# Kernel optimization log

Measured on AMD Instinct MI355X. Metric: run time of the kernel, lower is better.

Reference implementation:

```python
import jax, jax.numpy as jnp
import numpy as np

# ---- grid / frustum config (from default grid_config & data_config) ----
DB = (1.0, 60.0, 1.0)                 # dbound
OGH, OGW, DS = 256, 704, 16           # input size, downsample
FH, FW = OGH // DS, OGW // DS         # 16, 44
DEPTH = int(round((DB[1] - DB[0]) / DB[2]))  # 59 depth bins
NX0, NX1, NZ = 128, 128, 1            # BEV grid
DX = np.array([0.8, 0.8, 20.0], np.float32)
BX = np.array([-51.2 + 0.4, -51.2 + 0.4, 0.0], np.float32)  # row0 + dx/2


def _frustum():
    # (D, FH, FW, 3): pixel (u, v, depth)
    ds = jnp.broadcast_to(jnp.arange(DB[0], DB[1], DB[2], dtype=jnp.float32).reshape(-1, 1, 1), (DEPTH, FH, FW))
    xs = jnp.broadcast_to(jnp.linspace(0.0, OGW - 1.0, FW, dtype=jnp.float32).reshape(1, 1, FW), (DEPTH, FH, FW))
    ys = jnp.broadcast_to(jnp.linspace(0.0, OGH - 1.0, FH, dtype=jnp.float32).reshape(1, FH, 1), (DEPTH, FH, FW))
    return jnp.stack([xs, ys, ds], axis=-1)


def _geometry(rots, trans, intrins, post_rots, post_trans, bda):
    # pixel frustum -> ego-frame 3D points; (B, N, D, FH, FW, 3)
    pts = _frustum() - post_trans[:, :, None, None, None, :]
    pts = jnp.einsum('bnij,bndhwj->bndhwi', jnp.linalg.inv(post_rots), pts)
    pts = jnp.concatenate([pts[..., :2] * pts[..., 2:3], pts[..., 2:3]], axis=-1)
    comb = jnp.einsum('bnij,bnjk->bnik', rots, jnp.linalg.inv(intrins))
    pts = jnp.einsum('bnij,bndhwj->bndhwi', comb, pts) + trans[:, :, None, None, None, :]
    pts = jnp.einsum('bij,bndhwj->bndhwi', bda, pts)
    return pts


def _voxel_pool(geom, vol):
    # geom: (B,N,D,FH,FW,3), vol: (B,N,D,FH,FW,C) -> BEV (B, C*NZ, NX0, NX1)
    B, C = vol.shape[0], vol.shape[-1]
    gidx = jnp.floor((geom - (BX - DX / 2.0)) / DX).astype(jnp.int32)
    kept = ((gidx[..., 0] >= 0) & (gidx[..., 0] < NX0)
            & (gidx[..., 1] >= 0) & (gidx[..., 1] < NX1)
            & (gidx[..., 2] >= 0) & (gidx[..., 2] < NZ))
    bidx = jnp.broadcast_to(jnp.arange(B, dtype=jnp.int32).reshape(B, 1, 1, 1, 1), gidx.shape[:-1])
    flat = ((bidx * NZ + gidx[..., 2]) * NX0 + gidx[..., 0]) * NX1 + gidx[..., 1]
    nvox = B * NZ * NX0 * NX1
    flat = jnp.where(kept, flat, nvox).reshape(-1)      # dump bucket for culled pts
    feats = vol.reshape(-1, C)
    bev = jax.ops.segment_sum(feats, flat, num_segments=nvox + 1)[:nvox]
    bev = bev.reshape(B, NZ, NX0, NX1, C)
    bev = jnp.moveaxis(bev, -1, 2).reshape(B, NZ * C, NX0, NX1)  # z-major channel cat
    return bev


def setup_inputs() -> dict:
    key = jax.random.key(0)
    B, N, CIN, CT = 4, 6, 512, 64
    k1, k2 = jax.random.split(key, 2)
    x = jax.random.normal(k1, (B, N, CIN, FH, FW), dtype=jnp.float32)
    weight = jax.random.normal(k2, (DEPTH + CT, CIN), dtype=jnp.float32) * 0.02
    bias = jnp.zeros((DEPTH + CT,), dtype=jnp.float32)
    # cam->ego rotation (cam z forward -> ego x, cam x right -> ego -y, cam y down -> ego -z)
    Rcam = jnp.asarray(np.array([[0., 0., 1.], [-1., 0., 0.], [0., -1., 0.]], np.float32))
    rots = jnp.tile(Rcam, (B, N, 1, 1))
    trans = jnp.zeros((B, N, 3), dtype=jnp.float32)
    K = jnp.asarray(np.array([[600., 0., 352.], [0., 600., 128.], [0., 0., 1.]], np.float32))
    intrins = jnp.tile(K, (B, N, 1, 1))
    post_rots = jnp.tile(jnp.eye(3, dtype=jnp.float32), (B, N, 1, 1))
    post_trans = jnp.zeros((B, N, 3), dtype=jnp.float32)
    bda = jnp.tile(jnp.eye(3, dtype=jnp.float32), (B, 1, 1))
    return dict(x=x, rots=rots, trans=trans, intrins=intrins, post_rots=post_rots,
                post_trans=post_trans, bda=bda, weight=weight, bias=bias)


def reference(x, rots, trans, intrins, post_rots, post_trans, bda, weight, bias):
    # 1x1 depth/context head (eval mode): (B,N,Cin,H,W) -> (B,N,D+C,H,W)
    out = jnp.einsum('bnchw,oc->bnohw', x, weight) + bias[None, None, :, None, None]
    depth = jax.nn.softmax(out[:, :, :DEPTH], axis=2)      # (B,N,D,H,W)
    feat = out[:, :, DEPTH:]                               # (B,N,C,H,W)
    # depth-context outer product -> frustum volume (B,N,D,H,W,C)
    vol = jnp.einsum('bndhw,bnchw->bndhwc', depth, feat)
    geom = _geometry(rots, trans, intrins, post_rots, post_trans, bda)
    bev = _voxel_pool(geom, vol)                           # (B, C*NZ, 128, 128)
    return bev, depth
```

## Files before the change

### kernel.cpp

```cpp
#include <hip/hip_runtime.h>
#include <math.h>

#define CIN   512
#define NOUT  123
#define DEPN  59
#define CT    64
#define B_    4
#define N_    6
#define FH    16
#define FW    44
#define HW    704
#define NPIX  (B_*N_*HW)
#define NX    128
#define BEV_ELEMS (B_*CT*NX*NX)
#define DEPTH_OFF BEV_ELEMS

#define TDREC   40
#define WS_WB   1920
#define WS_PS   (WS_WB + 32768)
#define WS_FS   (WS_PS + NPIX*64)
#define WS_GC   (WS_FS + NPIX*64)

typedef short bf16x8 __attribute__((ext_vector_type(8)));
typedef float f32x4  __attribute__((ext_vector_type(4)));

__device__ inline unsigned short f2bf(float f) {
    unsigned u = __float_as_uint(f);
    return (unsigned short)((u + 0x7fffu + ((u >> 16) & 1u)) >> 16);
}

__device__ inline void inv3d(const double* m, double* o) {
    #pragma clang fp contract(off)
    double c00 = m[4]*m[8] - m[5]*m[7];
    double c01 = m[5]*m[6] - m[3]*m[8];
    double c02 = m[3]*m[7] - m[4]*m[6];
    double det = m[0]*c00 + m[1]*c01 + m[2]*c02;
    o[0] = c00/det; o[1] = (m[2]*m[7]-m[1]*m[8])/det; o[2] = (m[1]*m[5]-m[2]*m[4])/det;
    o[3] = c01/det; o[4] = (m[0]*m[8]-m[2]*m[6])/det; o[5] = (m[2]*m[3]-m[0]*m[5])/det;
    o[6] = c02/det; o[7] = (m[1]*m[6]-m[0]*m[7])/det; o[8] = (m[0]*m[4]-m[1]*m[3])/det;
}
__device__ inline void mm3d(const double* a, const double* b, double* o) {
    #pragma clang fp contract(off)
    for (int i = 0; i < 3; ++i)
        for (int k = 0; k < 3; ++k)
            o[i*3+k] = (a[i*3+0]*b[0*3+k] + a[i*3+1]*b[1*3+k]) + a[i*3+2]*b[2*3+k];
}

__global__ void k0_prep(const float* __restrict__ rots, const float* __restrict__ trans,
                        const float* __restrict__ intr, const float* __restrict__ prots,
                        const float* __restrict__ ptrans, const float* __restrict__ bda,
                        const float* __restrict__ W, float* __restrict__ ws,
                        float* __restrict__ dout) {
    int tid = blockIdx.x * 256 + threadIdx.x;
    int stride = gridDim.x * 256;
    float4 z = {0.f, 0.f, 0.f, 0.f};
    for (int i = tid; i < BEV_ELEMS / 4; i += stride)
        *(float4*)(dout + 4 * (size_t)i) = z;
    unsigned short* wb = (unsigned short*)(ws + WS_WB);
    for (int i = tid; i < 128 * CIN; i += stride) {
        int o = i >> 9, c = i & 511;
        wb[i] = (o < NOUT) ? f2bf(W[o * CIN + c]) : (unsigned short)0;
    }
    if (blockIdx.x == 0 && threadIdx.x < B_ * N_) {
        #pragma clang fp contract(off)
        int t = threadIdx.x;
        int b = t / N_;
        double* X = (double*)(ws) + t * TDREC;
        double PR[9], Kd[9], Rd[9], Bd[9];
        for (int i = 0; i < 9; ++i) PR[i] = (double)prots[t * 9 + i];
        for (int i = 0; i < 9; ++i) Kd[i] = (double)intr[t * 9 + i];
        for (int i = 0; i < 9; ++i) Rd[i] = (double)rots[t * 9 + i];
        for (int i = 0; i < 9; ++i) Bd[i] = (double)bda[b * 9 + i];
        double iPR[9]; inv3d(PR, iPR);
        for (int i = 0; i < 9; ++i) X[i] = iPR[i];
        for (int i = 0; i < 3; ++i) X[9 + i] = (double)ptrans[t * 3 + i];
        double iK[9];  inv3d(Kd, iK);
        double comb[9]; mm3d(Rd, iK, comb);
        for (int i = 0; i < 9; ++i) X[12 + i] = comb[i];
        for (int i = 0; i < 3; ++i) X[21 + i] = (double)trans[t * 3 + i];
        for (int i = 0; i < 9; ++i) X[24 + i] = Bd[i];
    }
}

__global__ __launch_bounds__(256) void k0b_coef(float* __restrict__ ws) {
    #pragma clang fp contract(off)
    int i = blockIdx.x * 256 + threadIdx.x;
    int b = i / (FW * 96);
    int rem = i - b * (FW * 96);
    int w = rem / 96;
    int j = rem - w * 96;
    int n = j >> 4, h = j & 15;
    const double* T = (const double*)(ws) + (b * N_ + n) * TDREC;
    const double xs = (w == 43) ? 703.0 : (double)w * (703.0 / 43.0);
    const double ys = (double)(h * 17);
    const double u0 = xs - T[9];
    const double u1 = ys - T[10];
    double pA[3], pB[3];
    #pragma unroll
    for (int k = 0; k < 3; ++k) {
        pA[k] = (T[3*k]*u0 + T[3*k+1]*u1) - T[3*k+2]*T[11];
        pB[k] = T[3*k+2];
    }
    double q0c[3] = { pA[0]*pA[2], pA[0]*pB[2] + pB[0]*pA[2], pB[0]*pB[2] };
    double q1c[3] = { pA[1]*pA[2], pA[1]*pB[2] + pB[1]*pA[2], pB[1]*pB[2] };
    double q2c[3] = { pA[2], pB[2], 0.0 };
    double rc[3][3], gc[3][3];
    #pragma unroll
    for (int r = 0; r < 3; ++r)
        #pragma unroll
        for (int k = 0; k < 3; ++k)
            rc[r][k] = ((T[12+3*r]*q0c[k] + T[13+3*r]*q1c[k]) + T[14+3*r]*q2c[k])
                       + ((k == 0) ? T[21+r] : 0.0);
    #pragma unroll
    for (int g = 0; g < 3; ++g)
        #pragma unroll
        for (int k = 0; k < 3; ++k)
            gc[g][k] = (T[24+3*g]*rc[0][k] + T[25+3*g]*rc[1][k]) + T[26+3*g]*rc[2][k];
    double* dst = (double*)(ws) + WS_GC / 2 + (size_t)i * 9;
    #pragma unroll
    for (int t = 0; t < 9; ++t) dst[t] = gc[t / 3][t % 3];
}

#define K1A   (64 * 72)
#define K1T   (K1A + 128 * 72)
__global__ __launch_bounds__(256, 2) void k1_gemm(const float* __restrict__ x,
                                                  const float* __restrict__ bias,
                                                  float* __restrict__ ws,
                                                  float* __restrict__ dout) {
    __shared__ __align__(16) unsigned short smem[2][K1T];
    const int tid = threadIdx.x;
    const int wave = tid >> 6, lane = tid & 63;
    const int l15 = lane & 15, quad = lane >> 4;
    const int bn = blockIdx.y;
    const int pixbase = blockIdx.x * 64;
    const float* xg = x + (size_t)bn * CIN * HW + pixbase;
    const unsigned short* wbg = (const unsigned short*)(ws + WS_WB);
    const int cpack = tid >> 4;
    const int pix4 = (tid & 15) * 4;
    const int wo  = tid >> 3;
    const int wsub = tid & 7;

    f32x4 acc[8] = {};
    float4 xr[2][4];
    uint4  wr[2][4];

    #pragma unroll
    for (int d = 0; d < 2; ++d) {
        const int ck = d * 64;
        const float* src = xg + (size_t)(ck + 4 * cpack) * HW + pix4;
        xr[d][0] = *(const float4*)(src);
        xr[d][1] = *(const float4*)(src + HW);
        xr[d][2] = *(const float4*)(src + 2 * HW);
        xr[d][3] = *(const float4*)(src + 3 * HW);
        #pragma unroll
        for (int i = 0; i < 4; ++i)
            wr[d][i] = *(const uint4*)(wbg + (size_t)(wo + 32 * i) * CIN + ck + wsub * 8);
    }

    #pragma unroll
    for (int it = 0; it < 8; ++it) {
        const int buf = it & 1;
        unsigned short* sa = smem[buf];
        unsigned short* sb = smem[buf] + K1A;
        {
            const float* f0 = (const float*)&xr[buf][0];
            const float* f1 = (const float*)&xr[buf][1];
            const float* f2 = (const float*)&xr[buf][2];
            const float* f3 = (const float*)&xr[buf][3];
            #pragma unroll
            for (int i = 0; i < 4; ++i) {
                uint2 pk;
                pk.x = (unsigned)f2bf(f0[i]) | ((unsigned)f2bf(f1[i]) << 16);
                pk.y = (unsigned)f2bf(f2[i]) | ((unsigned)f2bf(f3[i]) << 16);
                *(uint2*)&sa[(pix4 + i) * 72 + 4 * cpack] = pk;
            }
            #pragma unroll
            for (int i = 0; i < 4; ++i)
                *(uint4*)&sb[(wo + 32 * i) * 72 + wsub * 8] = wr[buf][i];
        }
        if (it < 6) {
            const int ck = (it + 2) * 64;
            const float* src = xg + (size_t)(ck + 4 * cpack) * HW + pix4;
            xr[buf][0] = *(const float4*)(src);
            xr[buf][1] = *(const float4*)(src + HW);
            xr[buf][2] = *(const float4*)(src + 2 * HW);
            xr[buf][3] = *(const float4*)(src + 3 * HW);
            #pragma unroll
            for (int i = 0; i < 4; ++i)
                wr[buf][i] = *(const uint4*)(wbg + (size_t)(wo + 32 * i) * CIN + ck + wsub * 8);
        }
        __syncthreads();
        #pragma unroll
        for (int ks = 0; ks < 64; ks += 32) {
            const bf16x8 a = *(const bf16x8*)&sa[(wave * 16 + l15) * 72 + ks + quad * 8];
            #pragma unroll
            for (int nt = 0; nt < 8; ++nt) {
                const bf16x8 b = *(const bf16x8*)&sb[(nt * 16 + l15) * 72 + ks + quad * 8];
                acc[nt] = __builtin_amdgcn_mfma_f32_16x16x32_bf16(a, b, acc[nt], 0, 0, 0);
            }
        }
    }

    float* sred = (float*)&smem[0][0];
    const int b = bn / N_, n = bn - b * N_;
    {
        float bb[8];
        #pragma unroll
        for (int nt = 0; nt < 8; ++nt) {
            int o = nt * 16 + l15;
            bb[nt] = (o < NOUT) ? bias[o] : 0.0f;
        }
        float* ps = ws + WS_PS;
        float* fs = ws + WS_FS;
        #pragma unroll
        for (int reg = 0; reg < 4; ++reg) {
            int pixl = wave * 16 + quad * 4 + reg;
            int pix = pixbase + pixl;
            int h = pix / FW, w = pix - h * FW;
            size_t row = (size_t)(b * FW + w) * 96 + n * FH + h;
            float v[4]; float m = -INFINITY;
            #pragma unroll
            for (int nt = 0; nt < 4; ++nt) {
                v[nt] = acc[nt][reg] + bb[nt];
                if (nt * 16 + l15 < DEPN) m = fmaxf(m, v[nt]);
            }
            #pragma unroll
            for (int msk = 8; msk >= 1; msk >>= 1) m = fmaxf(m, __shfl_xor(m, msk, 64));
            float e[4], s = 0.0f;
            #pragma unroll
            for (int nt = 0; nt < 4; ++nt) {
                e[nt] = (nt * 16 + l15 < DEPN) ? expf(v[nt] - m) : 0.0f;
                s += e[nt];
            }
            #pragma unroll
            for (int msk = 8; msk >= 1; msk >>= 1) s += __shfl_xor(s, msk, 64);
            const float inv = 1.0f / s;
            #pragma unroll
            for (int nt = 0; nt < 4; ++nt) {
                int o = nt * 16 + l15;
                if (o < DEPN) {
                    float p = e[nt] * inv;
                    ps[row * 64 + o] = p;
                    sred[pixl * 65 + o] = p;
                } else fs[row * 64 + (o - DEPN)] = v[nt];
            }
            #pragma unroll
            for (int nt = 4; nt < 8; ++nt) {
                int o = nt * 16 + l15;
                if (o < NOUT) fs[row * 64 + (o - DEPN)] = acc[nt][reg] + bb[nt];
            }
        }
    }
    __syncthreads();
    for (int o = wave; o < DEPN; o += 4)
        dout[DEPTH_OFF + ((size_t)bn * DEPN + o) * HW + pixbase + lane] = sred[lane * 65 + o];
}

#define DQ2 16
__global__ __launch_bounds__(256) void k2b_geom(float* __restrict__ ws,
                                                float* __restrict__ dout) {
    __shared__ float sF[96][64];
    __shared__ float sP[DQ2][100];
    __shared__ unsigned short sv16[DQ2 * 96];
    __shared__ __align__(16) double sG[96 * 9];
    __shared__ int sflag[DQ2];
    const int tid = threadIdx.x;
    const int bw = blockIdx.x;
    const int b = bw / FW;
    const int dbase = blockIdx.y * DQ2;
    const int nd = min(DQ2, DEPN - dbase);

    {
        const float* fsrc = ws + WS_FS + (size_t)bw * (96 * 64);
        const float* psrc = ws + WS_PS + (size_t)bw * (96 * 64);
        for (int i = tid; i < 96 * 16; i += 256) {
            int j = i >> 4, c4 = (i & 15) * 4;
            *(float4*)&sF[j][c4] = *(const float4*)(fsrc + j * 64 + c4);
        }
        for (int i = tid; i < 96 * 4; i += 256) {
            int j = i >> 2, q = i & 3;
            const float4 p4 = *(const float4*)(psrc + j * 64 + dbase + 4 * q);
            sP[4 * q + 0][j] = p4.x; sP[4 * q + 1][j] = p4.y;
            sP[4 * q + 2][j] = p4.z; sP[4 * q + 3][j] = p4.w;
        }
        const double2* gsrc = (const double2*)((const double*)(ws) + WS_GC / 2
                                               + (size_t)bw * (96 * 9));
        for (int i = tid; i < 432; i += 256)
            ((double2*)sG)[i] = gsrc[i];
    }
    __syncthreads();

    {
        const double BXY = (double)(-51.2000007629394531f);
        for (int idx = tid; idx < nd * 96; idx += 256) {
            int dl = idx / 96, j = idx - dl * 96;
            const double* G = &sG[j * 9];
            const double dsv = (double)(dbase + dl + 1);
            const double g0 = (G[2] * dsv + G[1]) * dsv + G[0];
            const double g1 = (G[5] * dsv + G[4]) * dsv + G[3];
            const double g2 = (G[8] * dsv + G[7]) * dsv + G[6];
            const double fx = floor((g0 - BXY) * 1.25);
            const double fy = floor((g1 - BXY) * 1.25);
            const bool keep = (fx >= 0.0) & (fx < 128.0) & (fy >= 0.0) & (fy < 128.0) &
                              (g2 >= -10.0) & (g2 < 10.0);
            sv16[idx] = keep ? (unsigned short)((int)fx * NX + (int)fy) : (unsigned short)0xFFFF;
        }
    }
    __syncthreads();

    {
        const int dl = tid >> 4, s = tid & 15;
        int u = -1, mix = 0;
        const int base = dl * 96 + s * 6;
        #pragma unroll
        for (int t = 0; t < 6; ++t) {
            int v = sv16[base + t];
            if (v != 0xFFFF) { if (u < 0) u = v; else if (v != u) mix = 1; }
        }
        #pragma unroll
        for (int msk = 1; msk < 16; msk <<= 1) {
            int uo = __shfl_xor(u, msk, 64);
            int mo = __shfl_xor(mix, msk, 64);
            mix = mix | mo | ((u >= 0 && uo >= 0 && uo != u) ? 1 : 0);
            u = (u < 0) ? uo : u;
        }
        if (s == 0 && dl < nd) sflag[dl] = mix ? -2 : u;
    }
    for (int idx = tid; idx < nd * 96; idx += 256) {
        if (sv16[idx] == 0xFFFF) {
            int dl = idx / 96, j = idx - dl * 96;
            sP[dl][j] = 0.0f;
        }
    }
    __syncthreads();

    const int dl = tid >> 4, ci = tid & 15;
    if (dl < nd && sflag[dl] >= 0) {
        float ax = 0.f, ay = 0.f, az = 0.f, aw = 0.f;
        for (int jj = 0; jj < 96; jj += 4) {
            const float4 pv = *(const float4*)&sP[dl][jj];
            const float4 f0 = *(const float4*)&sF[jj + 0][4 * ci];
            const float4 f1 = *(const float4*)&sF[jj + 1][4 * ci];
            const float4 f2 = *(const float4*)&sF[jj + 2][4 * ci];
            const float4 f3 = *(const float4*)&sF[jj + 3][4 * ci];
            ax = fmaf(pv.x, f0.x, ax); ay = fmaf(pv.x, f0.y, ay);
            az = fmaf(pv.x, f0.z, az); aw = fmaf(pv.x, f0.w, aw);
            ax = fmaf(pv.y, f1.x, ax); ay = fmaf(pv.y, f1.y, ay);
            az = fmaf(pv.y, f1.z, az); aw = fmaf(pv.y, f1.w, aw);
            ax = fmaf(pv.z, f2.x, ax); ay = fmaf(pv.z, f2.y, ay);
            az = fmaf(pv.z, f2.z, az); aw = fmaf(pv.z, f2.w, aw);
            ax = fmaf(pv.w, f3.x, ax); ay = fmaf(pv.w, f3.y, ay);
            az = fmaf(pv.w, f3.z, az); aw = fmaf(pv.w, f3.w, aw);
        }
        float* dst = dout + (((size_t)(b * CT + 4 * ci)) << 14) + sflag[dl];
        atomicAdd(dst,             ax);
        atomicAdd(dst + (1 << 14), ay);
        atomicAdd(dst + (2 << 14), az);
        atomicAdd(dst + (3 << 14), aw);
    }
    for (int d2 = 0; d2 < nd; ++d2) {
        if (sflag[d2] == -2) {
            int c = tid & 63, g = tid >> 6;
            for (int jj = 0; jj < 24; ++jj) {
                int j = g * 24 + jj;
                int v = sv16[d2 * 96 + j];
                if (v != 0xFFFF)
                    atomicAdd(dout + (((size_t)(b * CT + c)) << 14) + v,
                              sP[d2][j] * sF[j][c]);
            }
        }
    }
}

extern "C" void kernel_launch(void* const* d_in, const int* in_sizes, int n_in,
                              void* d_out, int out_size, void* d_ws, size_t ws_size,
                              hipStream_t stream) {
    const float* x      = (const float*)d_in[0];
    const float* rots   = (const float*)d_in[1];
    const float* trans  = (const float*)d_in[2];
    const float* intr   = (const float*)d_in[3];
    const float* prots  = (const float*)d_in[4];
    const float* ptrans = (const float*)d_in[5];
    const float* bda    = (const float*)d_in[6];
    const float* W      = (const float*)d_in[7];
    const float* bias   = (const float*)d_in[8];
    float* out = (float*)d_out;
    float* ws  = (float*)d_ws;

    k0_prep<<<512, 256, 0, stream>>>(rots, trans, intr, prots, ptrans, bda, W, ws, out);
    k0b_coef<<<66, 256, 0, stream>>>(ws);
    k1_gemm<<<dim3(HW / 64, B_ * N_), 256, 0, stream>>>(x, bias, ws, out);
    k2b_geom<<<dim3(B_ * FW, 4), 256, 0, stream>>>(ws, out);
}
```

Baseline: 163.0 us.

## Fuse all four kernels into one cooperative persistent kernel with grid syncs

Merges the prep, coefficient, GEMM and voxel-pool kernels into a single cooperative launch of 512 blocks separated by grid.sync(). The BEV zeroing moves onto the blocks left idle during the GEMM phase, the per-pixel geometry coefficients are now computed in shared memory per tile instead of round-tripping through a workspace buffer, and the GEMM prefetch goes from two-deep to one-deep register staging. The aim is to remove launch gaps and overlap the zeroing with the GEMM. In exchange it pays for grid-wide barriers and has lower occupancy limits with a single shared-memory buffer. The shallower prefetch may also expose more load latency.

Measured after the change: 274.0 us. 1.68x slower.

```diff
diff --git a/kernel.cpp b/kernel.cpp
--- a/kernel.cpp
+++ b/kernel.cpp
@@ -1,5 +1,8 @@
 #include <hip/hip_runtime.h>
+#include <hip/hip_cooperative_groups.h>
 #include <math.h>
+
+namespace cg = cooperative_groups;
 
 #define CIN   512
 #define NOUT  123
@@ -19,7 +22,10 @@
 #define WS_WB   1920
 #define WS_PS   (WS_WB + 32768)
 #define WS_FS   (WS_PS + NPIX*64)
-#define WS_GC   (WS_FS + NPIX*64)
+
+#define GRID    512
+#define K1TILES 264
+#define P2TILES (B_*FW*4)
 
 typedef short bf16x8 __attribute__((ext_vector_type(8)));
 typedef float f32x4  __attribute__((ext_vector_type(4)));
@@ -46,327 +52,324 @@
             o[i*3+k] = (a[i*3+0]*b[0*3+k] + a[i*3+1]*b[1*3+k]) + a[i*3+2]*b[2*3+k];
 }
 
-__global__ void k0_prep(const float* __restrict__ rots, const float* __restrict__ trans,
-                        const float* __restrict__ intr, const float* __restrict__ prots,
-                        const float* __restrict__ ptrans, const float* __restrict__ bda,
-                        const float* __restrict__ W, float* __restrict__ ws,
-                        float* __restrict__ dout) {
-    int tid = blockIdx.x * 256 + threadIdx.x;
-    int stride = gridDim.x * 256;
-    float4 z = {0.f, 0.f, 0.f, 0.f};
-    for (int i = tid; i < BEV_ELEMS / 4; i += stride)
-        *(float4*)(dout + 4 * (size_t)i) = z;
-    unsigned short* wb = (unsigned short*)(ws + WS_WB);
-    for (int i = tid; i < 128 * CIN; i += stride) {
-        int o = i >> 9, c = i & 511;
-        wb[i] = (o < NOUT) ? f2bf(W[o * CIN + c]) : (unsigned short)0;
+#define K1A   4608
+#define K1T   13824
+#define SMEM_BYTES 55296
+
+__global__ __launch_bounds__(256, 2) void fused(
+        const float* __restrict__ x,     const float* __restrict__ rots,
+        const float* __restrict__ trans, const float* __restrict__ intr,
+        const float* __restrict__ prots, const float* __restrict__ ptrans,
+        const float* __restrict__ bda,   const float* __restrict__ W,
+        const float* __restrict__ bias,  float* __restrict__ ws,
+        float* __restrict__ dout) {
+    __shared__ __align__(16) unsigned char smem[SMEM_BYTES];
+    cg::grid_group grid = cg::this_grid();
+    const int tid = threadIdx.x;
+    const int bid = blockIdx.x;
+
+    {
+        unsigned short* wb = (unsigned short*)(ws + WS_WB);
+        for (int i = bid * 256 + tid; i < 128 * CIN; i += GRID * 256) {
+            int o = i >> 9, c = i & 511;
+            wb[i] = (o < NOUT) ? f2bf(W[o * CIN + c]) : (unsigned short)0;
+        }
+        if (bid == 0 && tid < B_ * N_) {
+            #pragma clang fp contract(off)
+            int t = tid;
+            int b = t / N_;
+            double* X = (double*)(ws) + t * TDREC;
+            double PR[9], Kd[9], Rd[9], Bd[9];
+            for (int i = 0; i < 9; ++i) PR[i] = (double)prots[t * 9 + i];
+            for (int i = 0; i < 9; ++i) Kd[i] = (double)intr[t * 9 + i];
+            for (int i = 0; i < 9; ++i) Rd[i] = (double)rots[t * 9 + i];
+            for (int i = 0; i < 9; ++i) Bd[i] = (double)bda[b * 9 + i];
+            double iPR[9]; inv3d(PR, iPR);
+            for (int i = 0; i < 9; ++i) X[i] = iPR[i];
+            for (int i = 0; i < 3; ++i) X[9 + i] = (double)ptrans[t * 3 + i];
+            double iK[9];  inv3d(Kd, iK);
+            double comb[9]; mm3d(Rd, iK, comb);
+            for (int i = 0; i < 9; ++i) X[12 + i] = comb[i];
+            for (int i = 0; i < 3; ++i) X[21 + i] = (double)trans[t * 3 + i];
+            for (int i = 0; i < 9; ++i) X[24 + i] = Bd[i];
+        }
     }
-    if (blockIdx.x == 0 && threadIdx.x < B_ * N_) {
-        #pragma clang fp contract(off)
-        int t = threadIdx.x;
-        int b = t / N_;
-        double* X = (double*)(ws) + t * TDREC;
-        double PR[9], Kd[9], Rd[9], Bd[9];
-        for (int i = 0; i < 9; ++i) PR[i] = (double)prots[t * 9 + i];
-        for (int i = 0; i < 9; ++i) Kd[i] = (double)intr[t * 9 + i];
-        for (int i = 0; i < 9; ++i) Rd[i] = (double)rots[t * 9 + i];
-        for (int i = 0; i < 9; ++i) Bd[i] = (double)bda[b * 9 + i];
-        double iPR[9]; inv3d(PR, iPR);
-        for (int i = 0; i < 9; ++i) X[i] = iPR[i];
-        for (int i = 0; i < 3; ++i) X[9 + i] = (double)ptrans[t * 3 + i];
-        double iK[9];  inv3d(Kd, iK);
-        double comb[9]; mm3d(Rd, iK, comb);
-        for (int i = 0; i < 9; ++i) X[12 + i] = comb[i];
-        for (int i = 0; i < 3; ++i) X[21 + i] = (double)trans[t * 3 + i];
-        for (int i = 0; i < 9; ++i) X[24 + i] = Bd[i];
-    }
-}
-
-__global__ __launch_bounds__(256) void k0b_coef(float* __restrict__ ws) {
-    #pragma clang fp contract(off)
-    int i = blockIdx.x * 256 + threadIdx.x;
-    int b = i / (FW * 96);
-    int rem = i - b * (FW * 96);
-    int w = rem / 96;
-    int j = rem - w * 96;
-    int n = j >> 4, h = j & 15;
-    const double* T = (const double*)(ws) + (b * N_ + n) * TDREC;
-    const double xs = (w == 43) ? 703.0 : (double)w * (703.0 / 43.0);
-    const double ys = (double)(h * 17);
-    const double u0 = xs - T[9];
-    const double u1 = ys - T[10];
-    double pA[3], pB[3];
-    #pragma unroll
-    for (int k = 0; k < 3; ++k) {
-        pA[k] = (T[3*k]*u0 + T[3*k+1]*u1) - T[3*k+2]*T[11];
-        pB[k] = T[3*k+2];
-    }
-    double q0c[3] = { pA[0]*pA[2], pA[0]*pB[2] + pB[0]*pA[2], pB[0]*pB[2] };
-    double q1c[3] = { pA[1]*pA[2], pA[1]*pB[2] + pB[1]*pA[2], pB[1]*pB[2] };
-    double q2c[3] = { pA[2], pB[2], 0.0 };
-    double rc[3][3], gc[3][3];
-    #pragma unroll
-    for (int r = 0; r < 3; ++r)
-        #pragma unroll
-        for (int k = 0; k < 3; ++k)
-            rc[r][k] = ((T[12+3*r]*q0c[k] + T[13+3*r]*q1c[k]) + T[14+3*r]*q2c[k])
-                       + ((k == 0) ? T[21+r] : 0.0);
-    #pragma unroll
-    for (int g = 0; g < 3; ++g)
-        #pragma unroll
-        for (int k = 0; k < 3; ++k)
-            gc[g][k] = (T[24+3*g]*rc[0][k] + T[25+3*g]*rc[1][k]) + T[26+3*g]*rc[2][k];
-    double* dst = (double*)(ws) + WS_GC / 2 + (size_t)i * 9;
-    #pragma unroll
-    for (int t = 0; t < 9; ++t) dst[t] = gc[t / 3][t % 3];
-}
-
-#define K1A   (64 * 72)
-#define K1T   (K1A + 128 * 72)
-__global__ __launch_bounds__(256, 2) void k1_gemm(const float* __restrict__ x,
-                                                  const float* __restrict__ bias,
-                                                  float* __restrict__ ws,
-                                                  float* __restrict__ dout) {
-    __shared__ __align__(16) unsigned short smem[2][K1T];
-    const int tid = threadIdx.x;
-    const int wave = tid >> 6, lane = tid & 63;
-    const int l15 = lane & 15, quad = lane >> 4;
-    const int bn = blockIdx.y;
-    const int pixbase = blockIdx.x * 64;
-    const float* xg = x + (size_t)bn * CIN * HW + pixbase;
-    const unsigned short* wbg = (const unsigned short*)(ws + WS_WB);
-    const int cpack = tid >> 4;
-    const int pix4 = (tid & 15) * 4;
-    const int wo  = tid >> 3;
-    const int wsub = tid & 7;
-
-    f32x4 acc[8] = {};
-    float4 xr[2][4];
-    uint4  wr[2][4];
-
-    #pragma unroll
-    for (int d = 0; d < 2; ++d) {
-        const int ck = d * 64;
-        const float* src = xg + (size_t)(ck + 4 * cpack) * HW + pix4;
-        xr[d][0] = *(const float4*)(src);
-        xr[d][1] = *(const float4*)(src + HW);
-        xr[d][2] = *(const float4*)(src + 2 * HW);
-        xr[d][3] = *(const float4*)(src + 3 * HW);
-        #pragma unroll
-        for (int i = 0; i < 4; ++i)
-            wr[d][i] = *(const uint4*)(wbg + (size_t)(wo + 32 * i) * CIN + ck + wsub * 8);
-    }
-
-    #pragma unroll
-    for (int it = 0; it < 8; ++it) {
-        const int buf = it & 1;
-        unsigned short* sa = smem[buf];
-        unsigned short* sb = smem[buf] + K1A;
+    grid.sync();
+
+    if (bid < K1TILES) {
+        const int wave = tid >> 6, lane = tid & 63;
+        const int l15 = lane & 15, quad = lane >> 4;
+        const int bn = bid / 11;
+        const int pixbase = (bid - bn * 11) * 64;
+        const float* xg = x + (size_t)bn * CIN * HW + pixbase;
+        const unsigned short* wbg = (const unsigned short*)(ws + WS_WB);
+        const int cpack = tid >> 4;
+        const int pix4 = (tid & 15) * 4;
+        const int wo  = tid >> 3;
+        const int wsub = tid & 7;
+        unsigned short* s16 = (unsigned short*)smem;
+
+        f32x4 acc[8] = {};
+        float4 xr0, xr1, xr2, xr3;
+        uint4  wr4[4];
         {
-            const float* f0 = (const float*)&xr[buf][0];
-            const float* f1 = (const float*)&xr[buf][1];
-            const float* f2 = (const float*)&xr[buf][2];
-            const float* f3 = (const float*)&xr[buf][3];
-            #pragma unroll
-            for (int i = 0; i < 4; ++i) {
-                uint2 pk;
-                pk.x = (unsigned)f2bf(f0[i]) | ((unsigned)f2bf(f1[i]) << 16);
-                pk.y = (unsigned)f2bf(f2[i]) | ((unsigned)f2bf(f3[i]) << 16);
-                *(uint2*)&sa[(pix4 + i) * 72 + 4 * cpack] = pk;
-            }
+            const float* src = xg + (size_t)(4 * cpack) * HW + pix4;
+            xr0 = *(const float4*)(src);
+            xr1 = *(const float4*)(src + HW);
+            xr2 = *(const float4*)(src + 2 * HW);
+            xr3 = *(const float4*)(src + 3 * HW);
             #pragma unroll
             for (int i = 0; i < 4; ++i)
-                *(uint4*)&sb[(wo + 32 * i) * 72 + wsub * 8] = wr[buf][i];
-        }
-        if (it < 6) {
-            const int ck = (it + 2) * 64;
-            const float* src = xg + (size_t)(ck + 4 * cpack) * HW + pix4;
-            xr[buf][0] = *(const float4*)(src);
-            xr[buf][1] = *(const float4*)(src + HW);
-            xr[buf][2] = *(const float4*)(src + 2 * HW);
-            xr[buf][3] = *(const float4*)(src + 3 * HW);
+                wr4[i] = *(const uint4*)(wbg + (size_t)(wo + 32 * i) * CIN + wsub * 8);
+        }
+        #pragma unroll
+        for (int it = 0; it < 8; ++it) {
+            const int buf = it & 1;
+            unsigned short* sa = s16 + buf * K1T;
+            unsigned short* sb = sa + K1A;
+            {
+                const float* f0 = (const float*)&xr0; const float* f1 = (const float*)&xr1;
+                const float* f2 = (const float*)&xr2; const float* f3 = (const float*)&xr3;
+                #pragma unroll
+                for (int i = 0; i < 4; ++i) {
+                    uint2 pk;
+                    pk.x = (unsigned)f2bf(f0[i]) | ((unsigned)f2bf(f1[i]) << 16);
+                    pk.y = (unsigned)f2bf(f2[i]) | ((unsigned)f2bf(f3[i]) << 16);
+                    *(uint2*)&sa[(pix4 + i) * 72 + 4 * cpack] = pk;
+                }
+                #pragma unroll
+                for (int i = 0; i < 4; ++i)
+                    *(uint4*)&sb[(wo + 32 * i) * 72 + wsub * 8] = wr4[i];
+            }
+            if (it < 7) {
+                const int ck = (it + 1) * 64;
+                const float* src = xg + (size_t)(ck + 4 * cpack) * HW + pix4;
+                xr0 = *(const float4*)(src);
+                xr1 = *(const float4*)(src + HW);
+                xr2 = *(const float4*)(src + 2 * HW);
+                xr3 = *(const float4*)(src + 3 * HW);
+                #pragma unroll
+                for (int i = 0; i < 4; ++i)
+                    wr4[i] = *(const uint4*)(wbg + (size_t)(wo + 32 * i) * CIN + ck + wsub * 8);
+            }
+            __syncthreads();
             #pragma unroll
-            for (int i = 0; i < 4; ++i)
-                wr[buf][i] = *(const uint4*)(wbg + (size_t)(wo + 32 * i) * CIN + ck + wsub * 8);
-        }
-        __syncthreads();
-        #pragma unroll
-        for (int ks = 0; ks < 64; ks += 32) {
-            const bf16x8 a = *(const bf16x8*)&sa[(wave * 16 + l15) * 72 + ks + quad * 8];
+            for (int ks = 0; ks < 64; ks += 32) {
+                const bf16x8 a = *(const bf16x8*)&sa[(wave * 16 + l15) * 72 + ks + quad * 8];
+                #pragma unroll
+                for (int nt = 0; nt < 8; ++nt) {
+                    const bf16x8 b = *(const bf16x8*)&sb[(nt * 16 + l15) * 72 + ks + quad * 8];
+                    acc[nt] = __builtin_amdgcn_mfma_f32_16x16x32_bf16(a, b, acc[nt], 0, 0, 0);
+                }
+            }
+        }
+        float* sred = (float*)smem;
+        const int b = bn / N_, n = bn - b * N_;
+        {
+            float bb[8];
             #pragma unroll
             for (int nt = 0; nt < 8; ++nt) {
-                const bf16x8 b = *(const bf16x8*)&sb[(nt * 16 + l15) * 72 + ks + quad * 8];
-                acc[nt] = __builtin_amdgcn_mfma_f32_16x16x32_bf16(a, b, acc[nt], 0, 0, 0);
-            }
-        }
+                int o = nt * 16 + l15;
+                bb[nt] = (o < NOUT) ? bias[o] : 0.0f;
+            }
+            float* ps = ws + WS_PS;
+            float* fs = ws + WS_FS;
+            #pragma unroll
+            for (int reg = 0; reg < 4; ++reg) {
+                int pixl = wave * 16 + quad * 4 + reg;
+                int pix = pixbase + pixl;
+                int h = pix / FW, w = pix - h * FW;
+                size_t row = (size_t)(b * FW + w) * 96 + n * FH + h;
+                float v[4]; float m = -INFINITY;
+                #pragma unroll
+                for (int nt = 0; nt < 4; ++nt) {
+                    v[nt] = acc[nt][reg] + bb[nt];
+                    if (nt * 16 + l15 < DEPN) m = fmaxf(m, v[nt]);
+                }
+                #pragma unroll
+                for (int msk = 8; msk >= 1; msk >>= 1) m = fmaxf(m, __shfl_xor(m, msk, 64));
+                float e[4], s = 0.0f;
+                #pragma unroll
+                for (int nt = 0; nt < 4; ++nt) {
+                    e[nt] = (nt * 16 + l15 < DEPN) ? expf(v[nt] - m) : 0.0f;
+                    s += e[nt];
+                }
+                #pragma unroll
+                for (int msk = 8; msk >= 1; msk >>= 1) s += __shfl_xor(s, msk, 64);
+                const float inv = 1.0f / s;
+                #pragma unroll
+                for (int nt = 0; nt < 4; ++nt) {
+                    int o = nt * 16 + l15;
+                    if (o < DEPN) {
+                        float p = e[nt] * inv;
+                        ps[row * 64 + o] = p;
+                        sred[pixl * 65 + o] = p;
+                    } else fs[row * 64 + (o - DEPN)] = v[nt];
+                }
+                #pragma unroll
+                for (int nt = 4; nt < 8; ++nt) {
+                    int o = nt * 16 + l15;
+                    if (o < NOUT) fs[row * 64 + (o - DEPN)] = acc[nt][reg] + bb[nt];
+                }
+            }
+        }
+        __syncthreads();
+        for (int o = wave; o < DEPN; o += 4)
+            dout[DEPTH_OFF + ((size_t)bn * DEPN + o) * HW + pixbase + lane] = sred[lane * 65 + o];
+    } else {
+        float4 z = {0.f, 0.f, 0.f, 0.f};
+        for (int i = (bid - K1TILES) * 256 + tid; i < BEV_ELEMS / 4; i += (GRID - K1TILES) * 256)
+            *(float4*)(dout + 4 * (size_t)i) = z;
     }
-
-    float* sred = (float*)&smem[0][0];
-    const int b = bn / N_, n = bn - b * N_;
+    grid.sync();
+
     {
-        float bb[8];
-        #pragma unroll
-        for (int nt = 0; nt < 8; ++nt) {
-            int o = nt * 16 + l15;
-            bb[nt] = (o < NOUT) ? bias[o] : 0.0f;
-        }
-        float* ps = ws + WS_PS;
-        float* fs = ws + WS_FS;
-        #pragma unroll
-        for (int reg = 0; reg < 4; ++reg) {
-            int pixl = wave * 16 + quad * 4 + reg;
-            int pix = pixbase + pixl;
-            int h = pix / FW, w = pix - h * FW;
-            size_t row = (size_t)(b * FW + w) * 96 + n * FH + h;
-            float v[4]; float m = -INFINITY;
-            #pragma unroll
-            for (int nt = 0; nt < 4; ++nt) {
-                v[nt] = acc[nt][reg] + bb[nt];
-                if (nt * 16 + l15 < DEPN) m = fmaxf(m, v[nt]);
-            }
-            #pragma unroll
-            for (int msk = 8; msk >= 1; msk >>= 1) m = fmaxf(m, __shfl_xor(m, msk, 64));
-            float e[4], s = 0.0f;
-            #pragma unroll
-            for (int nt = 0; nt < 4; ++nt) {
-                e[nt] = (nt * 16 + l15 < DEPN) ? expf(v[nt] - m) : 0.0f;
-                s += e[nt];
-            }
-            #pragma unroll
-            for (int msk = 8; msk >= 1; msk >>= 1) s += __shfl_xor(s, msk, 64);
-            const float inv = 1.0f / s;
-            #pragma unroll
-            for (int nt = 0; nt < 4; ++nt) {
-                int o = nt * 16 + l15;
-                if (o < DEPN) {
-                    float p = e[nt] * inv;
-                    ps[row * 64 + o] = p;
-                    sred[pixl * 65 + o] = p;
-                } else fs[row * 64 + (o - DEPN)] = v[nt];
-            }
-            #pragma unroll
-            for (int nt = 4; nt < 8; ++nt) {
-                int o = nt * 16 + l15;
-                if (o < NOUT) fs[row * 64 + (o - DEPN)] = acc[nt][reg] + bb[nt];
-            }
-        }
-    }
-    __syncthreads();
-    for (int o = wave; o < DEPN; o += 4)
-        dout[DEPTH_OFF + ((size_t)bn * DEPN + o) * HW + pixbase + lane] = sred[lane * 65 + o];
-}
-
-#define DQ2 16
-__global__ __launch_bounds__(256) void k2b_geom(float* __restrict__ ws,
-                                                float* __restrict__ dout) {
-    __shared__ float sF[96][64];
-    __shared__ float sP[DQ2][100];
-    __shared__ unsigned short sv16[DQ2 * 96];
-    __shared__ __align__(16) double sG[96 * 9];
-    __shared__ int sflag[DQ2];
-    const int tid = threadIdx.x;
-    const int bw = blockIdx.x;
-    const int b = bw / FW;
-    const int dbase = blockIdx.y * DQ2;
-    const int nd = min(DQ2, DEPN - dbase);
-
-    {
-        const float* fsrc = ws + WS_FS + (size_t)bw * (96 * 64);
-        const float* psrc = ws + WS_PS + (size_t)bw * (96 * 64);
-        for (int i = tid; i < 96 * 16; i += 256) {
-            int j = i >> 4, c4 = (i & 15) * 4;
-            *(float4*)&sF[j][c4] = *(const float4*)(fsrc + j * 64 + c4);
-        }
-        for (int i = tid; i < 96 * 4; i += 256) {
-            int j = i >> 2, q = i & 3;
-            const float4 p4 = *(const float4*)(psrc + j * 64 + dbase + 4 * q);
-            sP[4 * q + 0][j] = p4.x; sP[4 * q + 1][j] = p4.y;
-            sP[4 * q + 2][j] = p4.z; sP[4 * q + 3][j] = p4.w;
-        }
-        const double2* gsrc = (const double2*)((const double*)(ws) + WS_GC / 2
-                                               + (size_t)bw * (96 * 9));
-        for (int i = tid; i < 432; i += 256)
-            ((double2*)sG)[i] = gsrc[i];
-    }
-    __syncthreads();
-
-    {
-        const double BXY = (double)(-51.2000007629394531f);
-        for (int idx = tid; idx < nd * 96; idx += 256) {
-            int dl = idx / 96, j = idx - dl * 96;
-            const double* G = &sG[j * 9];
-            const double dsv = (double)(dbase + dl + 1);
-            const double g0 = (G[2] * dsv + G[1]) * dsv + G[0];
-            const double g1 = (G[5] * dsv + G[4]) * dsv + G[3];
-            const double g2 = (G[8] * dsv + G[7]) * dsv + G[6];
-            const double fx = floor((g0 - BXY) * 1.25);
-            const double fy = floor((g1 - BXY) * 1.25);
-            const bool keep = (fx >= 0.0) & (fx < 128.0) & (fy >= 0.0) & (fy < 128.0) &
-                              (g2 >= -10.0) & (g2 < 10.0);
-            sv16[idx] = keep ? (unsigned short)((int)fx * NX + (int)fy) : (unsigned short)0xFFFF;
-        }
-    }
-    __syncthreads();
-
-    {
-        const int dl = tid >> 4, s = tid & 15;
-        int u = -1, mix = 0;
-        const int base = dl * 96 + s * 6;
-        #pragma unroll
-        for (int t = 0; t < 6; ++t) {
-            int v = sv16[base + t];
-            if (v != 0xFFFF) { if (u < 0) u = v; else if (v != u) mix = 1; }
-        }
-        #pragma unroll
-        for (int msk = 1; msk < 16; msk <<= 1) {
-            int uo = __shfl_xor(u, msk, 64);
-            int mo = __shfl_xor(mix, msk, 64);
-            mix = mix | mo | ((u >= 0 && uo >= 0 && uo != u) ? 1 : 0);
-            u = (u < 0) ? uo : u;
-        }
-        if (s == 0 && dl < nd) sflag[dl] = mix ? -2 : u;
-    }
-    for (int idx = tid; idx < nd * 96; idx += 256) {
-        if (sv16[idx] == 0xFFFF) {
-            int dl = idx / 96, j = idx - dl * 96;
-            sP[dl][j] = 0.0f;
-        }
-    }
-    __syncthreads();
-
-    const int dl = tid >> 4, ci = tid & 15;
-    if (dl < nd && sflag[dl] >= 0) {
-        float ax = 0.f, ay = 0.f, az = 0.f, aw = 0.f;
-        for (int jj = 0; jj < 96; jj += 4) {
-            const float4 pv = *(const float4*)&sP[dl][jj];
-            const float4 f0 = *(const float4*)&sF[jj + 0][4 * ci];
-            const float4 f1 = *(const float4*)&sF[jj + 1][4 * ci];
-            const float4 f2 = *(const float4*)&sF[jj + 2][4 * ci];
-            const float4 f3 = *(const float4*)&sF[jj + 3][4 * ci];
-            ax = fmaf(pv.x, f0.x, ax); ay = fmaf(pv.x, f0.y, ay);
-            az = fmaf(pv.x, f0.z, az); aw = fmaf(pv.x, f0.w, aw);
-            ax = fmaf(pv.y, f1.x, ax); ay = fmaf(pv.y, f1.y, ay);
-            az = fmaf(pv.y, f1.z, az); aw = fmaf(pv.y, f1.w, aw);
-            ax = fmaf(pv.z, f2.x, ax); ay = fmaf(pv.z, f2.y, ay);
-            az = fmaf(pv.z, f2.z, az); aw = fmaf(pv.z, f2.w, aw);
-            ax = fmaf(pv.w, f3.x, ax); ay = fmaf(pv.w, f3.y, ay);
-            az = fmaf(pv.w, f3.z, az); aw = fmaf(pv.w, f3.w, aw);
-        }
-        float* dst = dout + (((size_t)(b * CT + 4 * ci)) << 14) + sflag[dl];
-        atomicAdd(dst,             ax);
-        atomicAdd(dst + (1 << 14), ay);
-        atomicAdd(dst + (2 << 14), az);
-        atomicAdd(dst + (3 << 14), aw);
-    }
-    for (int d2 = 0; d2 < nd; ++d2) {
-        if (sflag[d2] == -2) {
-            int c = tid & 63, g = tid >> 6;
-            for (int jj = 0; jj < 24; ++jj) {
-                int j = g * 24 + jj;
-                int v = sv16[d2 * 96 + j];
-                if (v != 0xFFFF)
-                    atomicAdd(dout + (((size_t)(b * CT + c)) << 14) + v,
-                              sP[d2][j] * sF[j][c]);
+        float*  sF   = (float*)smem;
+        float*  sP   = (float*)(smem + 24576);
+        unsigned short* sv16 = (unsigned short*)(smem + 30976);
+        double* sG   = (double*)(smem + 34048);
+        double* sT   = (double*)(smem + 40960);
+        int*    sflag = (int*)(smem + 42880);
+
+        for (int t = bid; t < P2TILES; t += GRID) {
+            const int bw = t >> 2;
+            const int dch = t & 3;
+            const int b = bw / FW, w = bw - b * FW;
+            const int dbase = dch * 16;
+            const int nd = min(16, DEPN - dbase);
+            __syncthreads();
+
+            {
+                const float* fsrc = ws + WS_FS + (size_t)bw * (96 * 64);
+                const float* psrc = ws + WS_PS + (size_t)bw * (96 * 64);
+                for (int i = tid; i < 96 * 16; i += 256) {
+                    int j = i >> 4, c4 = (i & 15) * 4;
+                    *(float4*)&sF[j * 64 + c4] = *(const float4*)(fsrc + j * 64 + c4);
+                }
+                for (int i = tid; i < 96 * 4; i += 256) {
+                    int j = i >> 2, q = i & 3;
+                    const float4 p4 = *(const float4*)(psrc + j * 64 + dbase + 4 * q);
+                    sP[(4 * q + 0) * 100 + j] = p4.x; sP[(4 * q + 1) * 100 + j] = p4.y;
+                    sP[(4 * q + 2) * 100 + j] = p4.z; sP[(4 * q + 3) * 100 + j] = p4.w;
+                }
+                if (tid < N_ * TDREC) sT[tid] = ((const double*)ws)[b * (N_ * TDREC) + tid];
+            }
+            __syncthreads();
+
+            if (tid < 96) {
+                #pragma clang fp contract(off)
+                int j = tid, n = j >> 4, h = j & 15;
+                const double* T = &sT[n * TDREC];
+                const double xs = (w == 43) ? 703.0 : (double)w * (703.0 / 43.0);
+                const double ys = (double)(h * 17);
+                const double u0 = xs - T[9];
+                const double u1 = ys - T[10];
+                double pA[3], pB[3];
+                #pragma unroll
+                for (int k = 0; k < 3; ++k) {
+                    pA[k] = (T[3*k]*u0 + T[3*k+1]*u1) - T[3*k+2]*T[11];
+                    pB[k] = T[3*k+2];
+                }
+                double q0c[3] = { pA[0]*pA[2], pA[0]*pB[2] + pB[0]*pA[2], pB[0]*pB[2] };
+                double q1c[3] = { pA[1]*pA[2], pA[1]*pB[2] + pB[1]*pA[2], pB[1]*pB[2] };
+                double q2c[3] = { pA[2], pB[2], 0.0 };
+                double rc[3][3], gc[3][3];
+                #pragma unroll
+                for (int r = 0; r < 3; ++r)
+                    #pragma unroll
+                    for (int k = 0; k < 3; ++k)
+                        rc[r][k] = ((T[12+3*r]*q0c[k] + T[13+3*r]*q1c[k]) + T[14+3*r]*q2c[k])
+                                   + ((k == 0) ? T[21+r] : 0.0);
+                #pragma unroll
+                for (int g = 0; g < 3; ++g)
+                    #pragma unroll
+                    for (int k = 0; k < 3; ++k)
+                        gc[g][k] = (T[24+3*g]*rc[0][k] + T[25+3*g]*rc[1][k]) + T[26+3*g]*rc[2][k];
+                #pragma unroll
+                for (int q = 0; q < 9; ++q) sG[j * 9 + q] = gc[q / 3][q % 3];
+            }
+            __syncthreads();
+
+            {
+                const double BXY = (double)(-51.2000007629394531f);
+                for (int idx = tid; idx < nd * 96; idx += 256) {
+                    int dl = idx / 96, j = idx - dl * 96;
+                    const double* G = &sG[j * 9];
+                    const double dsv = (double)(dbase + dl + 1);
+                    const double g0 = (G[2] * dsv + G[1]) * dsv + G[0];
+                    const double g1 = (G[5] * dsv + G[4]) * dsv + G[3];
+                    const double g2 = (G[8] * dsv + G[7]) * dsv + G[6];
+                    const double fx = floor((g0 - BXY) * 1.25);
+                    const double fy = floor((g1 - BXY) * 1.25);
+                    const bool keep = (fx >= 0.0) & (fx < 128.0) & (fy >= 0.0) & (fy < 128.0) &
+                                      (g2 >= -10.0) & (g2 < 10.0);
+                    sv16[idx] = keep ? (unsigned short)((int)fx * NX + (int)fy)
+                                     : (unsigned short)0xFFFF;
+                }
+            }
+            __syncthreads();
+
+            {
+                const int dl = tid >> 4, s = tid & 15;
+                int u = -1, mix = 0;
+                const int base = dl * 96 + s * 6;
+                #pragma unroll
+                for (int q = 0; q < 6; ++q) {
+                    int v = sv16[base + q];
+                    if (v != 0xFFFF) { if (u < 0) u = v; else if (v != u) mix = 1; }
+                }
+                #pragma unroll
+                for (int msk = 1; msk < 16; msk <<= 1) {
+                    int uo = __shfl_xor(u, msk, 64);
+                    int mo = __shfl_xor(mix, msk, 64);
+                    mix = mix | mo | ((u >= 0 && uo >= 0 && uo != u) ? 1 : 0);
+                    u = (u < 0) ? uo : u;
+                }
+                if (s == 0 && dl < nd) sflag[dl] = mix ? -2 : u;
+            }
+            for (int idx = tid; idx < nd * 96; idx += 256) {
+                if (sv16[idx] == 0xFFFF) {
+                    int dl = idx / 96, j = idx - dl * 96;
+                    sP[dl * 100 + j] = 0.0f;
+                }
+            }
+            __syncthreads();
+
+            const int dl = tid >> 4, ci = tid & 15;
+            if (dl < nd && sflag[dl] >= 0) {
+                float ax = 0.f, ay = 0.f, az = 0.f, aw = 0.f;
+                for (int jj = 0; jj < 96; jj += 4) {
+                    const float4 pv = *(const float4*)&sP[dl * 100 + jj];
+                    const float4 f0 = *(const float4*)&sF[(jj + 0) * 64 + 4 * ci];
+                    const float4 f1 = *(const float4*)&sF[(jj + 1) * 64 + 4 * ci];
+                    const float4 f2 = *(const float4*)&sF[(jj + 2) * 64 + 4 * ci];
+                    const float4 f3 = *(const float4*)&sF[(jj + 3) * 64 + 4 * ci];
+                    ax = fmaf(pv.x, f0.x, ax); ay = fmaf(pv.x, f0.y, ay);
+                    az = fmaf(pv.x, f0.z, az); aw = fmaf(pv.x, f0.w, aw);
+                    ax = fmaf(pv.y, f1.x, ax); ay = fmaf(pv.y, f1.y, ay);
+                    az = fmaf(pv.y, f1.z, az); aw = fmaf(pv.y, f1.w, aw);
+                    ax = fmaf(pv.z, f2.x, ax); ay = fmaf(pv.z, f2.y, ay);
+                    az = fmaf(pv.z, f2.z, az); aw = fmaf(pv.z, f2.w, aw);
+                    ax = fmaf(pv.w, f3.x, ax); ay = fmaf(pv.w, f3.y, ay);
+                    az = fmaf(pv.w, f3.z, az); aw = fmaf(pv.w, f3.w, aw);
+                }
+                float* dst = dout + (((size_t)(b * CT + 4 * ci)) << 14) + sflag[dl];
+                atomicAdd(dst,             ax);
+                atomicAdd(dst + (1 << 14), ay);
+                atomicAdd(dst + (2 << 14), az);
+                atomicAdd(dst + (3 << 14), aw);
+            }
+            for (int d2 = 0; d2 < nd; ++d2) {
+                if (sflag[d2] == -2) {
+                    int c = tid & 63, g = tid >> 6;
+                    for (int jj = 0; jj < 24; ++jj) {
+                        int j = g * 24 + jj;
+                        int v = sv16[d2 * 96 + j];
+                        if (v != 0xFFFF)
+                            atomicAdd(dout + (((size_t)(b * CT + c)) << 14) + v,
+                                      sP[d2 * 100 + j] * sF[j * 64 + c]);
+                    }
+                }
             }
         }
     }
@@ -387,8 +390,6 @@
     float* out = (float*)d_out;
     float* ws  = (float*)d_ws;
 
-    k0_prep<<<512, 256, 0, stream>>>(rots, trans, intr, prots, ptrans, bda, W, ws, out);
-    k0b_coef<<<66, 256, 0, stream>>>(ws);
-    k1_gemm<<<dim3(HW / 64, B_ * N_), 256, 0, stream>>>(x, bias, ws, out);
-    k2b_geom<<<dim3(B_ * FW, 4), 256, 0, stream>>>(ws, out);
-}
+    void* args[] = { &x, &rots, &trans, &intr, &prots, &ptrans, &bda, &W, &bias, &ws, &out };
+    hipLaunchCooperativeKernel((void*)fused, dim3(GRID), dim3(256), args, 0, stream);
+}
```

## Fuse geometry coefficient kernel into prep and shrink GEMM prefetch depth

Applied to the files above, without the earlier changes.

Folds the per-camera transform setup and per-ray coefficient computation into the prep kernel. The first 66 blocks each rebuild the 24 camera transforms in shared memory and then compute their coefficients, which removes one kernel launch and the global round trip for the transform records. The GEMM kernel's register prefetch goes from two chunks ahead to one, cutting register pressure at the cost of less latency hiding for the global loads. Each of the 66 blocks now repeats the small matrix inversions.

New measurement: 157.5 us. 1.03x faster.

```diff
diff --git a/kernel.cpp b/kernel.cpp
--- a/kernel.cpp
+++ b/kernel.cpp
@@ -15,7 +15,6 @@
 #define BEV_ELEMS (B_*CT*NX*NX)
 #define DEPTH_OFF BEV_ELEMS
 
-#define TDREC   40
 #define WS_WB   1920
 #define WS_PS   (WS_WB + 32768)
 #define WS_FS   (WS_PS + NPIX*64)
@@ -46,26 +45,30 @@
             o[i*3+k] = (a[i*3+0]*b[0*3+k] + a[i*3+1]*b[1*3+k]) + a[i*3+2]*b[2*3+k];
 }
 
-__global__ void k0_prep(const float* __restrict__ rots, const float* __restrict__ trans,
-                        const float* __restrict__ intr, const float* __restrict__ prots,
-                        const float* __restrict__ ptrans, const float* __restrict__ bda,
-                        const float* __restrict__ W, float* __restrict__ ws,
-                        float* __restrict__ dout) {
-    int tid = blockIdx.x * 256 + threadIdx.x;
+__global__ __launch_bounds__(256) void k0_prep(
+        const float* __restrict__ rots,  const float* __restrict__ trans,
+        const float* __restrict__ intr,  const float* __restrict__ prots,
+        const float* __restrict__ ptrans,const float* __restrict__ bda,
+        const float* __restrict__ W,     float* __restrict__ ws,
+        float* __restrict__ dout) {
+    __shared__ double sTd[24][33];
+    const int tid = threadIdx.x;
+    const int bid = blockIdx.x;
+    int gtid = bid * 256 + tid;
     int stride = gridDim.x * 256;
     float4 z = {0.f, 0.f, 0.f, 0.f};
-    for (int i = tid; i < BEV_ELEMS / 4; i += stride)
+    for (int i = gtid; i < BEV_ELEMS / 4; i += stride)
         *(float4*)(dout + 4 * (size_t)i) = z;
     unsigned short* wb = (unsigned short*)(ws + WS_WB);
-    for (int i = tid; i < 128 * CIN; i += stride) {
+    for (int i = gtid; i < 128 * CIN; i += stride) {
         int o = i >> 9, c = i & 511;
         wb[i] = (o < NOUT) ? f2bf(W[o * CIN + c]) : (unsigned short)0;
     }
-    if (blockIdx.x == 0 && threadIdx.x < B_ * N_) {
+    if (bid >= 66) return;
+    if (tid < B_ * N_) {
         #pragma clang fp contract(off)
-        int t = threadIdx.x;
-        int b = t / N_;
-        double* X = (double*)(ws) + t * TDREC;
+        int t = tid, b = t / N_;
+        double* X = sTd[t];
         double PR[9], Kd[9], Rd[9], Bd[9];
         for (int i = 0; i < 9; ++i) PR[i] = (double)prots[t * 9 + i];
         for (int i = 0; i < 9; ++i) Kd[i] = (double)intr[t * 9 + i];
@@ -80,54 +83,54 @@
         for (int i = 0; i < 3; ++i) X[21 + i] = (double)trans[t * 3 + i];
         for (int i = 0; i < 9; ++i) X[24 + i] = Bd[i];
     }
-}
-
-__global__ __launch_bounds__(256) void k0b_coef(float* __restrict__ ws) {
-    #pragma clang fp contract(off)
-    int i = blockIdx.x * 256 + threadIdx.x;
-    int b = i / (FW * 96);
-    int rem = i - b * (FW * 96);
-    int w = rem / 96;
-    int j = rem - w * 96;
-    int n = j >> 4, h = j & 15;
-    const double* T = (const double*)(ws) + (b * N_ + n) * TDREC;
-    const double xs = (w == 43) ? 703.0 : (double)w * (703.0 / 43.0);
-    const double ys = (double)(h * 17);
-    const double u0 = xs - T[9];
-    const double u1 = ys - T[10];
-    double pA[3], pB[3];
-    #pragma unroll
-    for (int k = 0; k < 3; ++k) {
-        pA[k] = (T[3*k]*u0 + T[3*k+1]*u1) - T[3*k+2]*T[11];
-        pB[k] = T[3*k+2];
-    }
-    double q0c[3] = { pA[0]*pA[2], pA[0]*pB[2] + pB[0]*pA[2], pB[0]*pB[2] };
-    double q1c[3] = { pA[1]*pA[2], pA[1]*pB[2] + pB[1]*pA[2], pB[1]*pB[2] };
-    double q2c[3] = { pA[2], pB[2], 0.0 };
-    double rc[3][3], gc[3][3];
-    #pragma unroll
-    for (int r = 0; r < 3; ++r)
-        #pragma unroll
-        for (int k = 0; k < 3; ++k)
-            rc[r][k] = ((T[12+3*r]*q0c[k] + T[13+3*r]*q1c[k]) + T[14+3*r]*q2c[k])
-                       + ((k == 0) ? T[21+r] : 0.0);
-    #pragma unroll
-    for (int g = 0; g < 3; ++g)
-        #pragma unroll
-        for (int k = 0; k < 3; ++k)
-            gc[g][k] = (T[24+3*g]*rc[0][k] + T[25+3*g]*rc[1][k]) + T[26+3*g]*rc[2][k];
-    double* dst = (double*)(ws) + WS_GC / 2 + (size_t)i * 9;
-    #pragma unroll
-    for (int t = 0; t < 9; ++t) dst[t] = gc[t / 3][t % 3];
-}
-
-#define K1A   (64 * 72)
-#define K1T   (K1A + 128 * 72)
+    __syncthreads();
+    {
+        #pragma clang fp contract(off)
+        int i = bid * 256 + tid;
+        int b = i / (FW * 96);
+        int rem = i - b * (FW * 96);
+        int w = rem / 96;
+        int j = rem - w * 96;
+        int n = j >> 4, h = j & 15;
+        const double* T = sTd[b * N_ + n];
+        const double xs = (w == 43) ? 703.0 : (double)w * (703.0 / 43.0);
+        const double ys = (double)(h * 17);
+        const double u0 = xs - T[9];
+        const double u1 = ys - T[10];
+        double pA[3], pB[3];
+        #pragma unroll
+        for (int k = 0; k < 3; ++k) {
+            pA[k] = (T[3*k]*u0 + T[3*k+1]*u1) - T[3*k+2]*T[11];
+            pB[k] = T[3*k+2];
+        }
+        double q0c[3] = { pA[0]*pA[2], pA[0]*pB[2] + pB[0]*pA[2], pB[0]*pB[2] };
+        double q1c[3] = { pA[1]*pA[2], pA[1]*pB[2] + pB[1]*pA[2], pB[1]*pB[2] };
+        double q2c[3] = { pA[2], pB[2], 0.0 };
+        double rc[3][3], gc[3][3];
+        #pragma unroll
+        for (int r = 0; r < 3; ++r)
+            #pragma unroll
+            for (int k = 0; k < 3; ++k)
+                rc[r][k] = ((T[12+3*r]*q0c[k] + T[13+3*r]*q1c[k]) + T[14+3*r]*q2c[k])
+                           + ((k == 0) ? T[21+r] : 0.0);
+        #pragma unroll
+        for (int g = 0; g < 3; ++g)
+            #pragma unroll
+            for (int k = 0; k < 3; ++k)
+                gc[g][k] = (T[24+3*g]*rc[0][k] + T[25+3*g]*rc[1][k]) + T[26+3*g]*rc[2][k];
+        double* dst = (double*)(ws) + WS_GC / 2 + (size_t)i * 9;
+        #pragma unroll
+        for (int q = 0; q < 9; ++q) dst[q] = gc[q / 3][q % 3];
+    }
+}
+
+#define K1A   4608
+#define K1T   13824
 __global__ __launch_bounds__(256, 2) void k1_gemm(const float* __restrict__ x,
                                                   const float* __restrict__ bias,
                                                   float* __restrict__ ws,
                                                   float* __restrict__ dout) {
-    __shared__ __align__(16) unsigned short smem[2][K1T];
+    __shared__ __align__(16) unsigned short s16[2 * K1T];
     const int tid = threadIdx.x;
     const int wave = tid >> 6, lane = tid & 63;
     const int l15 = lane & 15, quad = lane >> 4;
@@ -141,32 +144,26 @@
     const int wsub = tid & 7;
 
     f32x4 acc[8] = {};
-    float4 xr[2][4];
-    uint4  wr[2][4];
-
-    #pragma unroll
-    for (int d = 0; d < 2; ++d) {
-        const int ck = d * 64;
-        const float* src = xg + (size_t)(ck + 4 * cpack) * HW + pix4;
-        xr[d][0] = *(const float4*)(src);
-        xr[d][1] = *(const float4*)(src + HW);
-        xr[d][2] = *(const float4*)(src + 2 * HW);
-        xr[d][3] = *(const float4*)(src + 3 * HW);
+    float4 xr0, xr1, xr2, xr3;
+    uint4  wr4[4];
+    {
+        const float* src = xg + (size_t)(4 * cpack) * HW + pix4;
+        xr0 = *(const float4*)(src);
+        xr1 = *(const float4*)(src + HW);
+        xr2 = *(const float4*)(src + 2 * HW);
+        xr3 = *(const float4*)(src + 3 * HW);
         #pragma unroll
         for (int i = 0; i < 4; ++i)
-            wr[d][i] = *(const uint4*)(wbg + (size_t)(wo + 32 * i) * CIN + ck + wsub * 8);
-    }
-
+            wr4[i] = *(const uint4*)(wbg + (size_t)(wo + 32 * i) * CIN + wsub * 8);
+    }
     #pragma unroll
     for (int it = 0; it < 8; ++it) {
         const int buf = it & 1;
-        unsigned short* sa = smem[buf];
-        unsigned short* sb = smem[buf] + K1A;
+        unsigned short* sa = s16 + buf * K1T;
+        unsigned short* sb = sa + K1A;
         {
-            const float* f0 = (const float*)&xr[buf][0];
-            const float* f1 = (const float*)&xr[buf][1];
-            const float* f2 = (const float*)&xr[buf][2];
-            const float* f3 = (const float*)&xr[buf][3];
+            const float* f0 = (const float*)&xr0; const float* f1 = (const float*)&xr1;
+            const float* f2 = (const float*)&xr2; const float* f3 = (const float*)&xr3;
             #pragma unroll
             for (int i = 0; i < 4; ++i) {
                 uint2 pk;
@@ -176,18 +173,18 @@
             }
             #pragma unroll
             for (int i = 0; i < 4; ++i)
-                *(uint4*)&sb[(wo + 32 * i) * 72 + wsub * 8] = wr[buf][i];
-        }
-        if (it < 6) {
-            const int ck = (it + 2) * 64;
+                *(uint4*)&sb[(wo + 32 * i) * 72 + wsub * 8] = wr4[i];
+        }
+        if (it < 7) {
+            const int ck = (it + 1) * 64;
             const float* src = xg + (size_t)(ck + 4 * cpack) * HW + pix4;
-            xr[buf][0] = *(const float4*)(src);
-            xr[buf][1] = *(const float4*)(src + HW);
-            xr[buf][2] = *(const float4*)(src + 2 * HW);
-            xr[buf][3] = *(const float4*)(src + 3 * HW);
+            xr0 = *(const float4*)(src);
+            xr1 = *(const float4*)(src + HW);
+            xr2 = *(const float4*)(src + 2 * HW);
+            xr3 = *(const float4*)(src + 3 * HW);
             #pragma unroll
             for (int i = 0; i < 4; ++i)
-                wr[buf][i] = *(const uint4*)(wbg + (size_t)(wo + 32 * i) * CIN + ck + wsub * 8);
+                wr4[i] = *(const uint4*)(wbg + (size_t)(wo + 32 * i) * CIN + ck + wsub * 8);
         }
         __syncthreads();
         #pragma unroll
@@ -200,8 +197,7 @@
             }
         }
     }
-
-    float* sred = (float*)&smem[0][0];
+    float* sred = (float*)s16;
     const int b = bn / N_, n = bn - b * N_;
     {
         float bb[8];
@@ -303,7 +299,8 @@
             const double fy = floor((g1 - BXY) * 1.25);
             const bool keep = (fx >= 0.0) & (fx < 128.0) & (fy >= 0.0) & (fy < 128.0) &
                               (g2 >= -10.0) & (g2 < 10.0);
-            sv16[idx] = keep ? (unsigned short)((int)fx * NX + (int)fy) : (unsigned short)0xFFFF;
+            sv16[idx] = keep ? (unsigned short)((int)fx * NX + (int)fy)
+                             : (unsigned short)0xFFFF;
         }
     }
     __syncthreads();
@@ -388,7 +385,6 @@
     float* ws  = (float*)d_ws;
 
     k0_prep<<<512, 256, 0, stream>>>(rots, trans, intr, prots, ptrans, bda, W, ws, out);
-    k0b_coef<<<66, 256, 0, stream>>>(ws);
     k1_gemm<<<dim3(HW / 64, B_ * N_), 256, 0, stream>>>(x, bias, ws, out);
     k2b_geom<<<dim3(B_ * FW, 4), 256, 0, stream>>>(ws, out);
 }
```
